# Kernel optimization log

Hardware: AMD Instinct MI355X
Metric: run time of the kernel (lower is better)

## Reference

```python
import jax, jax.numpy as jnp
import numpy as np

B, D, T, K = 32768, 1024, 100, 4  # batch, input_dim, num_trees, 2**(tree_depth-1)

def setup_inputs() -> dict:
    key = jax.random.key(0)
    k1, k2, k3, k4, k5 = jax.random.split(key, 5)
    s1 = 1.0 / np.sqrt(D)
    s2 = 1.0 / np.sqrt(K)
    return {
        "x": jax.random.normal(k1, (B, D), dtype=jnp.float32),
        "W1": jax.random.uniform(k2, (T, K, D), jnp.float32, -s1, s1),  # per-tree first Linear
        "b1": jax.random.uniform(k3, (T, K), jnp.float32, -s1, s1),
        "final_weight": jnp.full((T,), 1.0 / T, dtype=jnp.float32),
        "fc_w": jax.random.uniform(k4, (2, K), jnp.float32, -s2, s2),
        "fc_b": jax.random.uniform(k5, (2,), jnp.float32, -s2, s2),
    }

def reference(x, W1, b1, final_weight, fc_w, fc_b):
    # split_probs for all trees at once: [B, T, K]
    split = jnp.einsum("bd,tkd->btk", x, W1) + b1[None, :, :]
    leaf = jax.nn.sigmoid(split)  # tree[1] is Sigmoid applied to split_probs
    # sum(split.unsqueeze(1)*leaf.unsqueeze(2), -1) == leaf * sum_k(split)
    tree_out = leaf * jnp.sum(split, axis=-1, keepdims=True)  # [B, T, K]
    weighted = jnp.einsum("btk,t->bk", tree_out, final_weight)  # [B, K]
    logits = weighted @ fc_w.T + fc_b  # [B, 2]
    return logits
```

## Files before the change

### kernel.cpp

```cpp
#include <hip/hip_runtime.h>
#include <hip/hip_bf16.h>


typedef __bf16 bf16x8 __attribute__((ext_vector_type(8)));
typedef float f32x4 __attribute__((ext_vector_type(4)));

#define B_ROWS 32768
#define D_DIM  1024
#define N_COLS 400
#define NPAD   512
#define BM     64
#define BK     32
#define NCHUNK 32
#define THREADS 512
#define NTPW 4
#define MT   4

__device__ __forceinline__ unsigned short f2bf(float f) {
    unsigned int u = __float_as_uint(f);
    u += 0x7FFFu + ((u >> 16) & 1u);
    return (unsigned short)(u >> 16);
}
__device__ __forceinline__ unsigned int pk2(float a, float b) {
    return (unsigned int)f2bf(a) | ((unsigned int)f2bf(b) << 16);
}
__device__ __forceinline__ uint4 cvt8u(float4 a, float4 b) {
    uint4 u;
    u.x = pk2(a.x, a.y); u.y = pk2(a.z, a.w);
    u.z = pk2(b.x, b.y); u.w = pk2(b.z, b.w);
    return u;
}
__device__ __forceinline__ bf16x8 cvt8(float4 a, float4 b) {
    return __builtin_bit_cast(bf16x8, cvt8u(a, b));
}

__global__ void cvt_pad_bf16_kernel(const float* __restrict__ in,
                                    unsigned short* __restrict__ out) {
    size_t i = ((size_t)blockIdx.x * 256 + threadIdx.x) * 8;
    if (i < (size_t)N_COLS * D_DIM) {
        float4 v0 = *reinterpret_cast<const float4*>(in + i);
        float4 v1 = *reinterpret_cast<const float4*>(in + i + 4);
        *reinterpret_cast<uint4*>(out + i) = cvt8u(v0, v1);
    } else {
        uint4 z; z.x = z.y = z.z = z.w = 0u;
        *reinterpret_cast<uint4*>(out + i) = z;
    }
}

__device__ __forceinline__ void gl_lds16(const unsigned short* g,
                                         unsigned short* l) {
    __builtin_amdgcn_global_load_lds(
        (const __attribute__((address_space(1))) unsigned int*)g,
        (__attribute__((address_space(3))) unsigned int*)l,
        16, 0, 0);
}

#define FOR_N_(OP, m) OP(m,0) OP(m,1) OP(m,2) OP(m,3)
#define FOR_MN(OP) FOR_N_(OP,0) FOR_N_(OP,1) FOR_N_(OP,2) FOR_N_(OP,3)

#define DECL_ACC(m,n) f32x4 acc##m##n = {};
#define MFMA_MN(m,n) acc##m##n = __builtin_amdgcn_mfma_f32_16x16x32_bf16( \
        afr##m, bfr##n, acc##m##n, 0, 0, 0);

template <int MODE>
__global__ __launch_bounds__(THREADS, 2) void xgb_v13(
    const float* __restrict__ x,
    const void*  __restrict__ b_any,
    const float* __restrict__ b1,
    const float* __restrict__ fw,
    const float* __restrict__ fcw,
    const float* __restrict__ fcb,
    float* __restrict__ out)
{
    __shared__ __align__(16) unsigned short Abuf[2][BM * BK];
    __shared__ __align__(16) unsigned short Bbuf[2][NPAD * BK];
    __shared__ float Pbuf[BM * 8 * 2];

    const int tid  = threadIdx.x;
    const int wave = tid >> 6;
    const int lane = tid & 63;
    const int quad = lane >> 4;
    const int l15  = lane & 15;
    const int nf   = wave;
    const int row0 = blockIdx.x * BM;

    FOR_MN(DECL_ACC)

    if (MODE == 0) {
        const unsigned short* w1b = (const unsigned short*)b_any;

#define BDECL(t) const unsigned short* bsrc##t; int bdst##t; \
        { const int s_ = wave + 8 * (t); const int rb_ = s_ * 16 + (lane >> 2); \
          const int cc_ = ((lane & 3) - (rb_ >> 1)) & 3; \
          bsrc##t = w1b + (size_t)rb_ * D_DIM + cc_ * 8; \
          bdst##t = s_ * 512; }
        BDECL(0) BDECL(1) BDECL(2) BDECL(3)

#define STAGEB(kc, Bb) do { \
        gl_lds16(bsrc0 + (kc), (Bb) + bdst0); \
        gl_lds16(bsrc1 + (kc), (Bb) + bdst1); \
        gl_lds16(bsrc2 + (kc), (Bb) + bdst2); \
        gl_lds16(bsrc3 + (kc), (Bb) + bdst3); } while (0)

        const int slot = tid & 255;
        const int r0a = slot >> 2, c0a = slot & 3;
        const float* asrc0 = x + (size_t)(row0 + r0a) * D_DIM + c0a * 8;
        const int adst0 = r0a * 32 + ((c0a + (r0a >> 1)) & 3) * 8;
        float4 a0lo, a0hi, a1lo, a1hi;

#define LOADA0(kc) do { \
        a0lo = *reinterpret_cast<const float4*>(asrc0 + (kc));     \
        a0hi = *reinterpret_cast<const float4*>(asrc0 + (kc) + 4); } while (0)
#define LOADA1(kc) do { \
        a1lo = *reinterpret_cast<const float4*>(asrc0 + (kc));     \
        a1hi = *reinterpret_cast<const float4*>(asrc0 + (kc) + 4); } while (0)
#define WRITEA0(Ab) do { \
        *reinterpret_cast<uint4*>((Ab) + adst0) = cvt8u(a0lo, a0hi); } while (0)
#define WRITEA1(Ab) do { \
        *reinterpret_cast<uint4*>((Ab) + adst0) = cvt8u(a1lo, a1hi); } while (0)

#define LOAD_AFR(m) { const int row_ = (m) * 16 + l15; \
        const int p_ = (quad + (row_ >> 1)) & 3; \
        afr##m = *reinterpret_cast<const bf16x8*>(Ab_ + row_ * 32 + p_ * 8); }
#define LOAD_BFR(n) { const int row_ = (nf * NTPW + (n)) * 16 + l15; \
        const int p_ = (quad + (row_ >> 1)) & 3; \
        bfr##n = *reinterpret_cast<const bf16x8*>(Bb_ + row_ * 32 + p_ * 8); }

        STAGEB(0, Bbuf[0]);
        __builtin_amdgcn_sched_barrier(0);
        LOADA0(0);
        WRITEA0(Abuf[0]);
        __builtin_amdgcn_sched_barrier(0);
        LOADA1(BK);

        #pragma unroll 1
        for (int c = 0; c < NCHUNK; ++c) {
            const int cur = c & 1;
            const unsigned short* Ab_ = Abuf[cur];
            const unsigned short* Bb_ = Bbuf[cur];
            if (c == NCHUNK - 1) {
                asm volatile("s_waitcnt vmcnt(0)" ::: "memory");
            } else {
                asm volatile("s_waitcnt vmcnt(2)" ::: "memory");
            }
            asm volatile("s_waitcnt lgkmcnt(0)" ::: "memory");
            __builtin_amdgcn_s_barrier();
            __builtin_amdgcn_sched_barrier(0);
            if (c + 1 < NCHUNK) {
                STAGEB((c + 1) * BK, Bbuf[1 - cur]);
                __builtin_amdgcn_sched_barrier(0);
                if (c + 2 < NCHUNK) {
                    if (cur == 0) LOADA0((c + 2) * BK);
                    else          LOADA1((c + 2) * BK);
                }
                __builtin_amdgcn_sched_barrier(0);
            }
            {
                bf16x8 afr0, afr1, afr2, afr3;
                bf16x8 bfr0, bfr1, bfr2, bfr3;
                LOAD_AFR(0) LOAD_AFR(1) LOAD_AFR(2) LOAD_AFR(3)
                LOAD_BFR(0) LOAD_BFR(1) LOAD_BFR(2) LOAD_BFR(3)
                FOR_MN(MFMA_MN)
            }
            if (c + 1 < NCHUNK) {
                if (cur == 0) WRITEA1(Abuf[1]);
                else          WRITEA0(Abuf[0]);
            }
        }
    } else {
        const float* af = x + (size_t)(row0 + l15) * D_DIM + quad * 8;
#define PBF(n) const float* pbf##n; { \
        int r_ = (nf * NTPW + (n)) * 16 + l15; if (r_ > N_COLS - 1) r_ = 0; \
        pbf##n = (const float*)b_any + (size_t)r_ * D_DIM + quad * 8; }
        PBF(0) PBF(1) PBF(2) PBF(3)
        for (int step = 0; step < NCHUNK; ++step) {
            const int off = step * BK;
            bf16x8 afr0, afr1, afr2, afr3;
            bf16x8 bfr0, bfr1, bfr2, bfr3;
#define LAF2(m) afr##m = cvt8( \
            *reinterpret_cast<const float4*>(af + (size_t)(m) * 16 * D_DIM + off), \
            *reinterpret_cast<const float4*>(af + (size_t)(m) * 16 * D_DIM + off + 4));
#define LBF2(n) bfr##n = cvt8( \
            *reinterpret_cast<const float4*>(pbf##n + off), \
            *reinterpret_cast<const float4*>(pbf##n + off + 4));
            LAF2(0) LAF2(1) LAF2(2) LAF2(3)
            LBF2(0) LBF2(1) LBF2(2) LBF2(3)
            FOR_MN(MFMA_MN)
        }
    }

    const float fcw0 = fcw[l15 & 3];
    const float fcw1 = fcw[4 + (l15 & 3)];

#define PRE_N(n) \
    const int  col##n  = (nf * NTPW + (n)) * 16 + l15; \
    const bool ok##n   = (col##n < N_COLS); \
    const float bias##n = ok##n ? b1[ok##n ? col##n : 0] : 0.0f; \
    const float tw##n   = ok##n ? fw[ok##n ? (col##n >> 2) : 0] : 0.0f;
    PRE_N(0) PRE_N(1) PRE_N(2) PRE_N(3)

#define EPI_TERM(m,r,n) { \
        const float split_ = acc##m##n[r] + bias##n; \
        float s_ = split_; \
        s_ += __shfl_xor(s_, 1); \
        s_ += __shfl_xor(s_, 2); \
        const float leaf_ = 1.0f / (1.0f + __expf(-split_)); \
        const float val_ = tw##n * leaf_ * s_; \
        q0 += val_ * fcw0; q1 += val_ * fcw1; }

#define EPI_ONE(m,r) { \
        float q0 = 0.f, q1 = 0.f; \
        EPI_TERM(m,r,0) EPI_TERM(m,r,1) EPI_TERM(m,r,2) EPI_TERM(m,r,3) \
        q0 += __shfl_xor(q0, 1); q0 += __shfl_xor(q0, 2); \
        q0 += __shfl_xor(q0, 4); q0 += __shfl_xor(q0, 8); \
        q1 += __shfl_xor(q1, 1); q1 += __shfl_xor(q1, 2); \
        q1 += __shfl_xor(q1, 4); q1 += __shfl_xor(q1, 8); \
        const int row_ = (m) * 16 + quad * 4 + (r);            \
        if (l15 == 0) Pbuf[(row_ * 8 + nf) * 2 + 0] = q0; \
        if (l15 == 1) Pbuf[(row_ * 8 + nf) * 2 + 1] = q1; }

#define EPI_M(m) EPI_ONE(m,0) EPI_ONE(m,1) EPI_ONE(m,2) EPI_ONE(m,3)
    EPI_M(0) EPI_M(1) EPI_M(2) EPI_M(3)

    __syncthreads();

    if (tid < 2 * BM) {
        const int r = tid >> 1, j = tid & 1;
        float s = fcb[j];
        #pragma unroll
        for (int w = 0; w < 8; ++w)
            s += Pbuf[(r * 8 + w) * 2 + j];
        out[(row0 + r) * 2 + j] = s;
    }
}

extern "C" void kernel_launch(void* const* d_in, const int* in_sizes, int n_in,
                              void* d_out, int out_size, void* d_ws, size_t ws_size,
                              hipStream_t stream) {
    const float* x   = (const float*)d_in[0];
    const float* W1  = (const float*)d_in[1];
    const float* b1  = (const float*)d_in[2];
    const float* fw  = (const float*)d_in[3];
    const float* fcw = (const float*)d_in[4];
    const float* fcb = (const float*)d_in[5];
    float* out = (float*)d_out;

    const size_t pad_elems = (size_t)NPAD * D_DIM;
    if (ws_size >= pad_elems * sizeof(unsigned short)) {
        unsigned short* w1b = (unsigned short*)d_ws;
        cvt_pad_bf16_kernel<<<(int)(pad_elems / 2048), 256, 0, stream>>>(W1, w1b);
        xgb_v13<0><<<B_ROWS / BM, THREADS, 0, stream>>>(
            x, (const void*)w1b, b1, fw, fcw, fcb, out);
    } else {
        xgb_v13<2><<<B_ROWS / BM, THREADS, 0, stream>>>(
            x, (const void*)W1, b1, fw, fcw, fcb, out);
    }
}
```

Before: 276.2 us.

## Enlarge block tile to 128x448 with 64-wide K chunks and 2x4 wave grid

Each block now covers 128 rows and 64-wide K chunks, instead of 64 rows and 32-wide chunks. The eight waves form a 2x4 grid, with each wave computing 4x7 MFMA tiles over a W1 pad shrunk from 512 to 448 columns. This is meant to cut W1 staging per output row, drop most of the wasted padded columns, and halve the number of loop iterations and barriers. The LDS swizzles are rewritten for 64-wide rows, and the x conversion stores now sit before the MFMA loop. The cost is a much larger LDS footprint (about 148 KB) that likely allows only one block per CU, plus higher register pressure from 28 accumulators.

New measurement: 229.4 us. -16.9%, faster.

```diff
diff --git a/kernel.cpp b/kernel.cpp
--- a/kernel.cpp
+++ b/kernel.cpp
@@ -8,12 +8,12 @@
 #define B_ROWS 32768
 #define D_DIM  1024
 #define N_COLS 400
-#define NPAD   512
-#define BM     64
-#define BK     32
-#define NCHUNK 32
+#define NPAD   448
+#define BM     128
+#define BK     64
+#define NCHUNK 16
 #define THREADS 512
-#define NTPW 4
+#define NTPW 7
 #define MT   4
 
 __device__ __forceinline__ unsigned short f2bf(float f) {
@@ -55,7 +55,7 @@
         16, 0, 0);
 }
 
-#define FOR_N_(OP, m) OP(m,0) OP(m,1) OP(m,2) OP(m,3)
+#define FOR_N_(OP, m) OP(m,0) OP(m,1) OP(m,2) OP(m,3) OP(m,4) OP(m,5) OP(m,6)
 #define FOR_MN(OP) FOR_N_(OP,0) FOR_N_(OP,1) FOR_N_(OP,2) FOR_N_(OP,3)
 
 #define DECL_ACC(m,n) f32x4 acc##m##n = {};
@@ -63,7 +63,7 @@
         afr##m, bfr##n, acc##m##n, 0, 0, 0);
 
 template <int MODE>
-__global__ __launch_bounds__(THREADS, 2) void xgb_v13(
+__global__ __launch_bounds__(THREADS, 2) void xgb_v14(
     const float* __restrict__ x,
     const void*  __restrict__ b_any,
     const float* __restrict__ b1,
@@ -74,14 +74,15 @@
 {
     __shared__ __align__(16) unsigned short Abuf[2][BM * BK];
     __shared__ __align__(16) unsigned short Bbuf[2][NPAD * BK];
-    __shared__ float Pbuf[BM * 8 * 2];
+    __shared__ float Pbuf[BM * 4 * 2];
 
     const int tid  = threadIdx.x;
     const int wave = tid >> 6;
     const int lane = tid & 63;
     const int quad = lane >> 4;
     const int l15  = lane & 15;
-    const int nf   = wave;
+    const int mh   = wave >> 2;
+    const int nf   = wave & 3;
     const int row0 = blockIdx.x * BM;
 
     FOR_MN(DECL_ACC)
@@ -90,48 +91,59 @@
         const unsigned short* w1b = (const unsigned short*)b_any;
 
 #define BDECL(t) const unsigned short* bsrc##t; int bdst##t; \
-        { const int s_ = wave + 8 * (t); const int rb_ = s_ * 16 + (lane >> 2); \
-          const int cc_ = ((lane & 3) - (rb_ >> 1)) & 3; \
-          bsrc##t = w1b + (size_t)rb_ * D_DIM + cc_ * 8; \
+        { const int s_ = wave + 8 * (t); const int rr_ = lane >> 3; \
+          const int cc_ = ((lane & 7) - rr_) & 7; \
+          bsrc##t = w1b + (size_t)(s_ * 8 + rr_) * D_DIM + cc_ * 8; \
           bdst##t = s_ * 512; }
-        BDECL(0) BDECL(1) BDECL(2) BDECL(3)
+        BDECL(0) BDECL(1) BDECL(2) BDECL(3) BDECL(4) BDECL(5) BDECL(6)
 
 #define STAGEB(kc, Bb) do { \
         gl_lds16(bsrc0 + (kc), (Bb) + bdst0); \
         gl_lds16(bsrc1 + (kc), (Bb) + bdst1); \
         gl_lds16(bsrc2 + (kc), (Bb) + bdst2); \
-        gl_lds16(bsrc3 + (kc), (Bb) + bdst3); } while (0)
-
-        const int slot = tid & 255;
-        const int r0a = slot >> 2, c0a = slot & 3;
+        gl_lds16(bsrc3 + (kc), (Bb) + bdst3); \
+        gl_lds16(bsrc4 + (kc), (Bb) + bdst4); \
+        gl_lds16(bsrc5 + (kc), (Bb) + bdst5); \
+        gl_lds16(bsrc6 + (kc), (Bb) + bdst6); } while (0)
+
+        const int r0a = tid >> 3, c0a = tid & 7;
         const float* asrc0 = x + (size_t)(row0 + r0a) * D_DIM + c0a * 8;
-        const int adst0 = r0a * 32 + ((c0a + (r0a >> 1)) & 3) * 8;
-        float4 a0lo, a0hi, a1lo, a1hi;
-
-#define LOADA0(kc) do { \
-        a0lo = *reinterpret_cast<const float4*>(asrc0 + (kc));     \
-        a0hi = *reinterpret_cast<const float4*>(asrc0 + (kc) + 4); } while (0)
-#define LOADA1(kc) do { \
-        a1lo = *reinterpret_cast<const float4*>(asrc0 + (kc));     \
-        a1hi = *reinterpret_cast<const float4*>(asrc0 + (kc) + 4); } while (0)
-#define WRITEA0(Ab) do { \
-        *reinterpret_cast<uint4*>((Ab) + adst0) = cvt8u(a0lo, a0hi); } while (0)
-#define WRITEA1(Ab) do { \
-        *reinterpret_cast<uint4*>((Ab) + adst0) = cvt8u(a1lo, a1hi); } while (0)
-
-#define LOAD_AFR(m) { const int row_ = (m) * 16 + l15; \
-        const int p_ = (quad + (row_ >> 1)) & 3; \
-        afr##m = *reinterpret_cast<const bf16x8*>(Ab_ + row_ * 32 + p_ * 8); }
+        const float* asrc1 = asrc0 + (size_t)64 * D_DIM;
+        const int adst0 = r0a * 64 + ((c0a + r0a) & 7) * 8;
+        float4 aX0lo, aX0hi, aX1lo, aX1hi;
+        float4 aY0lo, aY0hi, aY1lo, aY1hi;
+
+#define LOADA_X(kc) do { \
+        aX0lo = *reinterpret_cast<const float4*>(asrc0 + (kc));     \
+        aX0hi = *reinterpret_cast<const float4*>(asrc0 + (kc) + 4); \
+        aX1lo = *reinterpret_cast<const float4*>(asrc1 + (kc));     \
+        aX1hi = *reinterpret_cast<const float4*>(asrc1 + (kc) + 4); } while (0)
+#define LOADA_Y(kc) do { \
+        aY0lo = *reinterpret_cast<const float4*>(asrc0 + (kc));     \
+        aY0hi = *reinterpret_cast<const float4*>(asrc0 + (kc) + 4); \
+        aY1lo = *reinterpret_cast<const float4*>(asrc1 + (kc));     \
+        aY1hi = *reinterpret_cast<const float4*>(asrc1 + (kc) + 4); } while (0)
+#define WRITEA_X(Ab) do { \
+        *reinterpret_cast<uint4*>((Ab) + adst0)        = cvt8u(aX0lo, aX0hi); \
+        *reinterpret_cast<uint4*>((Ab) + adst0 + 4096) = cvt8u(aX1lo, aX1hi); \
+        } while (0)
+#define WRITEA_Y(Ab) do { \
+        *reinterpret_cast<uint4*>((Ab) + adst0)        = cvt8u(aY0lo, aY0hi); \
+        *reinterpret_cast<uint4*>((Ab) + adst0 + 4096) = cvt8u(aY1lo, aY1hi); \
+        } while (0)
+
+#define LOAD_AFR(m) { const int row_ = mh * 64 + (m) * 16 + l15; \
+        const int p_ = (quad + h * 4 + row_) & 7; \
+        afr##m = *reinterpret_cast<const bf16x8*>(Ab_ + row_ * 64 + p_ * 8); }
 #define LOAD_BFR(n) { const int row_ = (nf * NTPW + (n)) * 16 + l15; \
-        const int p_ = (quad + (row_ >> 1)) & 3; \
-        bfr##n = *reinterpret_cast<const bf16x8*>(Bb_ + row_ * 32 + p_ * 8); }
-
+        const int p_ = (quad + h * 4 + row_) & 7; \
+        bfr##n = *reinterpret_cast<const bf16x8*>(Bb_ + row_ * 64 + p_ * 8); }
+
+        LOADA_X(0);
+        WRITEA_X(Abuf[0]);
         STAGEB(0, Bbuf[0]);
         __builtin_amdgcn_sched_barrier(0);
-        LOADA0(0);
-        WRITEA0(Abuf[0]);
-        __builtin_amdgcn_sched_barrier(0);
-        LOADA1(BK);
+        LOADA_Y(BK);
 
         #pragma unroll 1
         for (int c = 0; c < NCHUNK; ++c) {
@@ -141,7 +153,7 @@
             if (c == NCHUNK - 1) {
                 asm volatile("s_waitcnt vmcnt(0)" ::: "memory");
             } else {
-                asm volatile("s_waitcnt vmcnt(2)" ::: "memory");
+                asm volatile("s_waitcnt vmcnt(4)" ::: "memory");
             }
             asm volatile("s_waitcnt lgkmcnt(0)" ::: "memory");
             __builtin_amdgcn_s_barrier();
@@ -149,34 +161,34 @@
             if (c + 1 < NCHUNK) {
                 STAGEB((c + 1) * BK, Bbuf[1 - cur]);
                 __builtin_amdgcn_sched_barrier(0);
+                if (cur == 0) WRITEA_Y(Abuf[1]);
+                else          WRITEA_X(Abuf[0]);
                 if (c + 2 < NCHUNK) {
-                    if (cur == 0) LOADA0((c + 2) * BK);
-                    else          LOADA1((c + 2) * BK);
+                    if (cur == 0) LOADA_X((c + 2) * BK);
+                    else          LOADA_Y((c + 2) * BK);
                 }
                 __builtin_amdgcn_sched_barrier(0);
             }
-            {
+            #pragma unroll
+            for (int h = 0; h < 2; ++h) {
                 bf16x8 afr0, afr1, afr2, afr3;
-                bf16x8 bfr0, bfr1, bfr2, bfr3;
+                bf16x8 bfr0, bfr1, bfr2, bfr3, bfr4, bfr5, bfr6;
                 LOAD_AFR(0) LOAD_AFR(1) LOAD_AFR(2) LOAD_AFR(3)
                 LOAD_BFR(0) LOAD_BFR(1) LOAD_BFR(2) LOAD_BFR(3)
+                LOAD_BFR(4) LOAD_BFR(5) LOAD_BFR(6)
                 FOR_MN(MFMA_MN)
-            }
-            if (c + 1 < NCHUNK) {
-                if (cur == 0) WRITEA1(Abuf[1]);
-                else          WRITEA0(Abuf[0]);
             }
         }
     } else {
-        const float* af = x + (size_t)(row0 + l15) * D_DIM + quad * 8;
+        const float* af = x + (size_t)(row0 + mh * 64 + l15) * D_DIM + quad * 8;
 #define PBF(n) const float* pbf##n; { \
         int r_ = (nf * NTPW + (n)) * 16 + l15; if (r_ > N_COLS - 1) r_ = 0; \
         pbf##n = (const float*)b_any + (size_t)r_ * D_DIM + quad * 8; }
-        PBF(0) PBF(1) PBF(2) PBF(3)
-        for (int step = 0; step < NCHUNK; ++step) {
-            const int off = step * BK;
+        PBF(0) PBF(1) PBF(2) PBF(3) PBF(4) PBF(5) PBF(6)
+        for (int step = 0; step < 32; ++step) {
+            const int off = step * 32;
             bf16x8 afr0, afr1, afr2, afr3;
-            bf16x8 bfr0, bfr1, bfr2, bfr3;
+            bf16x8 bfr0, bfr1, bfr2, bfr3, bfr4, bfr5, bfr6;
 #define LAF2(m) afr##m = cvt8( \
             *reinterpret_cast<const float4*>(af + (size_t)(m) * 16 * D_DIM + off), \
             *reinterpret_cast<const float4*>(af + (size_t)(m) * 16 * D_DIM + off + 4));
@@ -184,7 +196,7 @@
             *reinterpret_cast<const float4*>(pbf##n + off), \
             *reinterpret_cast<const float4*>(pbf##n + off + 4));
             LAF2(0) LAF2(1) LAF2(2) LAF2(3)
-            LBF2(0) LBF2(1) LBF2(2) LBF2(3)
+            LBF2(0) LBF2(1) LBF2(2) LBF2(3) LBF2(4) LBF2(5) LBF2(6)
             FOR_MN(MFMA_MN)
         }
     }
@@ -197,7 +209,7 @@
     const bool ok##n   = (col##n < N_COLS); \
     const float bias##n = ok##n ? b1[ok##n ? col##n : 0] : 0.0f; \
     const float tw##n   = ok##n ? fw[ok##n ? (col##n >> 2) : 0] : 0.0f;
-    PRE_N(0) PRE_N(1) PRE_N(2) PRE_N(3)
+    PRE_N(0) PRE_N(1) PRE_N(2) PRE_N(3) PRE_N(4) PRE_N(5) PRE_N(6)
 
 #define EPI_TERM(m,r,n) { \
         const float split_ = acc##m##n[r] + bias##n; \
@@ -211,13 +223,14 @@
 #define EPI_ONE(m,r) { \
         float q0 = 0.f, q1 = 0.f; \
         EPI_TERM(m,r,0) EPI_TERM(m,r,1) EPI_TERM(m,r,2) EPI_TERM(m,r,3) \
+        EPI_TERM(m,r,4) EPI_TERM(m,r,5) EPI_TERM(m,r,6) \
         q0 += __shfl_xor(q0, 1); q0 += __shfl_xor(q0, 2); \
         q0 += __shfl_xor(q0, 4); q0 += __shfl_xor(q0, 8); \
         q1 += __shfl_xor(q1, 1); q1 += __shfl_xor(q1, 2); \
         q1 += __shfl_xor(q1, 4); q1 += __shfl_xor(q1, 8); \
-        const int row_ = (m) * 16 + quad * 4 + (r);            \
-        if (l15 == 0) Pbuf[(row_ * 8 + nf) * 2 + 0] = q0; \
-        if (l15 == 1) Pbuf[(row_ * 8 + nf) * 2 + 1] = q1; }
+        const int row_ = mh * 64 + (m) * 16 + quad * 4 + (r);    \
+        if (l15 == 0) Pbuf[(row_ * 4 + nf) * 2 + 0] = q0; \
+        if (l15 == 1) Pbuf[(row_ * 4 + nf) * 2 + 1] = q1; }
 
 #define EPI_M(m) EPI_ONE(m,0) EPI_ONE(m,1) EPI_ONE(m,2) EPI_ONE(m,3)
     EPI_M(0) EPI_M(1) EPI_M(2) EPI_M(3)
@@ -228,8 +241,8 @@
         const int r = tid >> 1, j = tid & 1;
         float s = fcb[j];
         #pragma unroll
-        for (int w = 0; w < 8; ++w)
-            s += Pbuf[(r * 8 + w) * 2 + j];
+        for (int w = 0; w < 4; ++w)
+            s += Pbuf[(r * 4 + w) * 2 + j];
         out[(row0 + r) * 2 + j] = s;
     }
 }
@@ -249,10 +262,10 @@
     if (ws_size >= pad_elems * sizeof(unsigned short)) {
         unsigned short* w1b = (unsigned short*)d_ws;
         cvt_pad_bf16_kernel<<<(int)(pad_elems / 2048), 256, 0, stream>>>(W1, w1b);
-        xgb_v13<0><<<B_ROWS / BM, THREADS, 0, stream>>>(
+        xgb_v14<0><<<B_ROWS / BM, THREADS, 0, stream>>>(
             x, (const void*)w1b, b1, fw, fcw, fcb, out);
     } else {
-        xgb_v13<2><<<B_ROWS / BM, THREADS, 0, stream>>>(
+        xgb_v14<2><<<B_ROWS / BM, THREADS, 0, stream>>>(
             x, (const void*)W1, b1, fw, fcw, fcb, out);
     }
 }
```

## Split output columns across two blocks and combine partial logits atomically

Applied to the files above, without the earlier changes.

The 400 tree columns are split into two 224-wide halves, each handled by its own 256-thread block, so the grid doubles and the padded width shrinks from 512 to 448. Each wave now computes a 32x112 tile, and the per-block partial logits are added into a zero-initialised output with atomicAdd, with each half contributing half the bias. The hand-tuned vmcnt waits and the two-deep A prefetch are replaced with a simple __syncthreads single-stage prefetch. The intent is less wasted padding work and more resident blocks per CU. In exchange the x tile is read twice, the change adds a memset launch and atomics, and it gives up the finer load/compute overlap.

Measured after the change: 270.7 us. 2.0% less time.

```diff
diff --git a/kernel.cpp b/kernel.cpp
--- a/kernel.cpp
+++ b/kernel.cpp
@@ -8,13 +8,14 @@
 #define B_ROWS 32768
 #define D_DIM  1024
 #define N_COLS 400
-#define NPAD   512
+#define NPAD   448
 #define BM     64
+#define BN     224
 #define BK     32
 #define NCHUNK 32
-#define THREADS 512
-#define NTPW 4
-#define MT   4
+#define THREADS 256
+#define NTPW 7
+#define MT   2
 
 __device__ __forceinline__ unsigned short f2bf(float f) {
     unsigned int u = __float_as_uint(f);
@@ -55,15 +56,15 @@
         16, 0, 0);
 }
 
-#define FOR_N_(OP, m) OP(m,0) OP(m,1) OP(m,2) OP(m,3)
-#define FOR_MN(OP) FOR_N_(OP,0) FOR_N_(OP,1) FOR_N_(OP,2) FOR_N_(OP,3)
+#define FOR_N_(OP, m) OP(m,0) OP(m,1) OP(m,2) OP(m,3) OP(m,4) OP(m,5) OP(m,6)
+#define FOR_MN(OP) FOR_N_(OP,0) FOR_N_(OP,1)
 
 #define DECL_ACC(m,n) f32x4 acc##m##n = {};
 #define MFMA_MN(m,n) acc##m##n = __builtin_amdgcn_mfma_f32_16x16x32_bf16( \
         afr##m, bfr##n, acc##m##n, 0, 0, 0);
 
 template <int MODE>
-__global__ __launch_bounds__(THREADS, 2) void xgb_v13(
+__global__ __launch_bounds__(THREADS, 3) void xgb_v15(
     const float* __restrict__ x,
     const void*  __restrict__ b_any,
     const float* __restrict__ b1,
@@ -73,16 +74,20 @@
     float* __restrict__ out)
 {
     __shared__ __align__(16) unsigned short Abuf[2][BM * BK];
-    __shared__ __align__(16) unsigned short Bbuf[2][NPAD * BK];
-    __shared__ float Pbuf[BM * 8 * 2];
+    __shared__ __align__(16) unsigned short Bbuf[2][BN * BK];
+    __shared__ float Pbuf[BM * 2 * 2];
 
     const int tid  = threadIdx.x;
     const int wave = tid >> 6;
     const int lane = tid & 63;
     const int quad = lane >> 4;
     const int l15  = lane & 15;
-    const int nf   = wave;
-    const int row0 = blockIdx.x * BM;
+    const int mh   = wave >> 1;
+    const int nf   = wave & 1;
+    const int mb   = blockIdx.x >> 1;
+    const int nh   = blockIdx.x & 1;
+    const int row0 = mb * BM;
+    const int bcol0 = nh * BN;
 
     FOR_MN(DECL_ACC)
 
@@ -90,101 +95,82 @@
         const unsigned short* w1b = (const unsigned short*)b_any;
 
 #define BDECL(t) const unsigned short* bsrc##t; int bdst##t; \
-        { const int s_ = wave + 8 * (t); const int rb_ = s_ * 16 + (lane >> 2); \
-          const int cc_ = ((lane & 3) - (rb_ >> 1)) & 3; \
-          bsrc##t = w1b + (size_t)rb_ * D_DIM + cc_ * 8; \
-          bdst##t = s_ * 512; }
+        { const int s_ = wave + 4 * (t); \
+          const int rb_ = s_ * 16 + (lane >> 2); \
+          const int rc_ = (s_ < 14) ? rb_ : 0;         \
+          const int cc_ = ((lane & 3) - (rc_ >> 1)) & 3; \
+          bsrc##t = w1b + (size_t)(bcol0 + rc_) * D_DIM + cc_ * 8; \
+          bdst##t = (s_ < 14 ? s_ : 0) * 512; }
         BDECL(0) BDECL(1) BDECL(2) BDECL(3)
 
 #define STAGEB(kc, Bb) do { \
         gl_lds16(bsrc0 + (kc), (Bb) + bdst0); \
         gl_lds16(bsrc1 + (kc), (Bb) + bdst1); \
         gl_lds16(bsrc2 + (kc), (Bb) + bdst2); \
-        gl_lds16(bsrc3 + (kc), (Bb) + bdst3); } while (0)
-
-        const int slot = tid & 255;
-        const int r0a = slot >> 2, c0a = slot & 3;
+        if (wave < 2) gl_lds16(bsrc3 + (kc), (Bb) + bdst3); } while (0)
+
+        const int r0a = tid >> 2, c0a = tid & 3;
         const float* asrc0 = x + (size_t)(row0 + r0a) * D_DIM + c0a * 8;
         const int adst0 = r0a * 32 + ((c0a + (r0a >> 1)) & 3) * 8;
-        float4 a0lo, a0hi, a1lo, a1hi;
-
-#define LOADA0(kc) do { \
-        a0lo = *reinterpret_cast<const float4*>(asrc0 + (kc));     \
-        a0hi = *reinterpret_cast<const float4*>(asrc0 + (kc) + 4); } while (0)
-#define LOADA1(kc) do { \
-        a1lo = *reinterpret_cast<const float4*>(asrc0 + (kc));     \
-        a1hi = *reinterpret_cast<const float4*>(asrc0 + (kc) + 4); } while (0)
-#define WRITEA0(Ab) do { \
-        *reinterpret_cast<uint4*>((Ab) + adst0) = cvt8u(a0lo, a0hi); } while (0)
-#define WRITEA1(Ab) do { \
-        *reinterpret_cast<uint4*>((Ab) + adst0) = cvt8u(a1lo, a1hi); } while (0)
-
-#define LOAD_AFR(m) { const int row_ = (m) * 16 + l15; \
+        float4 areg0, areg1;
+
+#define LOADA(kc) do { \
+        areg0 = *reinterpret_cast<const float4*>(asrc0 + (kc));     \
+        areg1 = *reinterpret_cast<const float4*>(asrc0 + (kc) + 4); } while (0)
+#define WRITEA(Ab) do { \
+        *reinterpret_cast<uint4*>((Ab) + adst0) = cvt8u(areg0, areg1); \
+        } while (0)
+
+#define LOAD_AFR(m) { const int row_ = mh * 32 + (m) * 16 + l15; \
         const int p_ = (quad + (row_ >> 1)) & 3; \
         afr##m = *reinterpret_cast<const bf16x8*>(Ab_ + row_ * 32 + p_ * 8); }
 #define LOAD_BFR(n) { const int row_ = (nf * NTPW + (n)) * 16 + l15; \
         const int p_ = (quad + (row_ >> 1)) & 3; \
         bfr##n = *reinterpret_cast<const bf16x8*>(Bb_ + row_ * 32 + p_ * 8); }
 
+        LOADA(0);
         STAGEB(0, Bbuf[0]);
-        __builtin_amdgcn_sched_barrier(0);
-        LOADA0(0);
-        WRITEA0(Abuf[0]);
-        __builtin_amdgcn_sched_barrier(0);
-        LOADA1(BK);
+        WRITEA(Abuf[0]);
 
         #pragma unroll 1
         for (int c = 0; c < NCHUNK; ++c) {
             const int cur = c & 1;
             const unsigned short* Ab_ = Abuf[cur];
             const unsigned short* Bb_ = Bbuf[cur];
-            if (c == NCHUNK - 1) {
-                asm volatile("s_waitcnt vmcnt(0)" ::: "memory");
-            } else {
-                asm volatile("s_waitcnt vmcnt(2)" ::: "memory");
-            }
-            asm volatile("s_waitcnt lgkmcnt(0)" ::: "memory");
-            __builtin_amdgcn_s_barrier();
-            __builtin_amdgcn_sched_barrier(0);
+            __syncthreads();
             if (c + 1 < NCHUNK) {
+                LOADA((c + 1) * BK);
                 STAGEB((c + 1) * BK, Bbuf[1 - cur]);
-                __builtin_amdgcn_sched_barrier(0);
-                if (c + 2 < NCHUNK) {
-                    if (cur == 0) LOADA0((c + 2) * BK);
-                    else          LOADA1((c + 2) * BK);
-                }
-                __builtin_amdgcn_sched_barrier(0);
             }
             {
-                bf16x8 afr0, afr1, afr2, afr3;
-                bf16x8 bfr0, bfr1, bfr2, bfr3;
-                LOAD_AFR(0) LOAD_AFR(1) LOAD_AFR(2) LOAD_AFR(3)
+                bf16x8 afr0, afr1;
+                bf16x8 bfr0, bfr1, bfr2, bfr3, bfr4, bfr5, bfr6;
+                LOAD_AFR(0) LOAD_AFR(1)
                 LOAD_BFR(0) LOAD_BFR(1) LOAD_BFR(2) LOAD_BFR(3)
+                LOAD_BFR(4) LOAD_BFR(5) LOAD_BFR(6)
                 FOR_MN(MFMA_MN)
             }
-            if (c + 1 < NCHUNK) {
-                if (cur == 0) WRITEA1(Abuf[1]);
-                else          WRITEA0(Abuf[0]);
-            }
+            if (c + 1 < NCHUNK) WRITEA(Abuf[1 - cur]);
         }
     } else {
-        const float* af = x + (size_t)(row0 + l15) * D_DIM + quad * 8;
+        const float* af = x + (size_t)(row0 + mh * 32 + l15) * D_DIM + quad * 8;
 #define PBF(n) const float* pbf##n; { \
-        int r_ = (nf * NTPW + (n)) * 16 + l15; if (r_ > N_COLS - 1) r_ = 0; \
+        int r_ = bcol0 + (nf * NTPW + (n)) * 16 + l15; \
+        if (r_ > N_COLS - 1) r_ = 0; \
         pbf##n = (const float*)b_any + (size_t)r_ * D_DIM + quad * 8; }
-        PBF(0) PBF(1) PBF(2) PBF(3)
+        PBF(0) PBF(1) PBF(2) PBF(3) PBF(4) PBF(5) PBF(6)
         for (int step = 0; step < NCHUNK; ++step) {
             const int off = step * BK;
-            bf16x8 afr0, afr1, afr2, afr3;
-            bf16x8 bfr0, bfr1, bfr2, bfr3;
+            bf16x8 afr0, afr1;
+            bf16x8 bfr0, bfr1, bfr2, bfr3, bfr4, bfr5, bfr6;
 #define LAF2(m) afr##m = cvt8( \
             *reinterpret_cast<const float4*>(af + (size_t)(m) * 16 * D_DIM + off), \
             *reinterpret_cast<const float4*>(af + (size_t)(m) * 16 * D_DIM + off + 4));
 #define LBF2(n) bfr##n = cvt8( \
             *reinterpret_cast<const float4*>(pbf##n + off), \
             *reinterpret_cast<const float4*>(pbf##n + off + 4));
-            LAF2(0) LAF2(1) LAF2(2) LAF2(3)
-            LBF2(0) LBF2(1) LBF2(2) LBF2(3)
+            LAF2(0) LAF2(1)
+            LBF2(0) LBF2(1) LBF2(2) LBF2(3) LBF2(4) LBF2(5) LBF2(6)
             FOR_MN(MFMA_MN)
         }
     }
@@ -193,11 +179,11 @@
     const float fcw1 = fcw[4 + (l15 & 3)];
 
 #define PRE_N(n) \
-    const int  col##n  = (nf * NTPW + (n)) * 16 + l15; \
+    const int  col##n  = bcol0 + (nf * NTPW + (n)) * 16 + l15; \
     const bool ok##n   = (col##n < N_COLS); \
     const float bias##n = ok##n ? b1[ok##n ? col##n : 0] : 0.0f; \
     const float tw##n   = ok##n ? fw[ok##n ? (col##n >> 2) : 0] : 0.0f;
-    PRE_N(0) PRE_N(1) PRE_N(2) PRE_N(3)
+    PRE_N(0) PRE_N(1) PRE_N(2) PRE_N(3) PRE_N(4) PRE_N(5) PRE_N(6)
 
 #define EPI_TERM(m,r,n) { \
         const float split_ = acc##m##n[r] + bias##n; \
@@ -211,26 +197,26 @@
 #define EPI_ONE(m,r) { \
         float q0 = 0.f, q1 = 0.f; \
         EPI_TERM(m,r,0) EPI_TERM(m,r,1) EPI_TERM(m,r,2) EPI_TERM(m,r,3) \
+        EPI_TERM(m,r,4) EPI_TERM(m,r,5) EPI_TERM(m,r,6) \
         q0 += __shfl_xor(q0, 1); q0 += __shfl_xor(q0, 2); \
         q0 += __shfl_xor(q0, 4); q0 += __shfl_xor(q0, 8); \
         q1 += __shfl_xor(q1, 1); q1 += __shfl_xor(q1, 2); \
         q1 += __shfl_xor(q1, 4); q1 += __shfl_xor(q1, 8); \
-        const int row_ = (m) * 16 + quad * 4 + (r);            \
-        if (l15 == 0) Pbuf[(row_ * 8 + nf) * 2 + 0] = q0; \
-        if (l15 == 1) Pbuf[(row_ * 8 + nf) * 2 + 1] = q1; }
+        const int row_ = mh * 32 + (m) * 16 + quad * 4 + (r);    \
+        if (l15 == 0) Pbuf[(row_ * 2 + nf) * 2 + 0] = q0; \
+        if (l15 == 1) Pbuf[(row_ * 2 + nf) * 2 + 1] = q1; }
 
 #define EPI_M(m) EPI_ONE(m,0) EPI_ONE(m,1) EPI_ONE(m,2) EPI_ONE(m,3)
-    EPI_M(0) EPI_M(1) EPI_M(2) EPI_M(3)
+    EPI_M(0) EPI_M(1)
 
     __syncthreads();
 
     if (tid < 2 * BM) {
         const int r = tid >> 1, j = tid & 1;
-        float s = fcb[j];
-        #pragma unroll
-        for (int w = 0; w < 8; ++w)
-            s += Pbuf[(r * 8 + w) * 2 + j];
-        out[(row0 + r) * 2 + j] = s;
+        float s = 0.5f * fcb[j]
+                + Pbuf[(r * 2 + 0) * 2 + j]
+                + Pbuf[(r * 2 + 1) * 2 + j];
+        atomicAdd(&out[(size_t)(row0 + r) * 2 + j], s);
     }
 }
 
@@ -245,14 +231,16 @@
     const float* fcb = (const float*)d_in[5];
     float* out = (float*)d_out;
 
+    hipMemsetAsync(out, 0, (size_t)B_ROWS * 2 * sizeof(float), stream);
+
     const size_t pad_elems = (size_t)NPAD * D_DIM;
     if (ws_size >= pad_elems * sizeof(unsigned short)) {
         unsigned short* w1b = (unsigned short*)d_ws;
         cvt_pad_bf16_kernel<<<(int)(pad_elems / 2048), 256, 0, stream>>>(W1, w1b);
-        xgb_v13<0><<<B_ROWS / BM, THREADS, 0, stream>>>(
+        xgb_v15<0><<<(B_ROWS / BM) * 2, THREADS, 0, stream>>>(
             x, (const void*)w1b, b1, fw, fcw, fcb, out);
     } else {
-        xgb_v13<2><<<B_ROWS / BM, THREADS, 0, stream>>>(
+        xgb_v15<2><<<(B_ROWS / BM) * 2, THREADS, 0, stream>>>(
             x, (const void*)W1, b1, fw, fcw, fcb, out);
     }
 }
```

## Warp-specialize GEMM into producer and consumer waves with 4-slot LDS ring

Applied to the files above, without the earlier changes.

Splits the 8 waves into 4 producer waves that stage x (converted to bf16) and W1 tiles into a 4-deep LDS ring, and 4 consumer waves that run MFMAs. Handshakes use LDS atomic counters and spin-waits instead of block barriers. Padding of the N dimension drops from 512 to 448 columns, so each consumer wave covers 7 column tiles and less padded MFMA work is done. The goal is deeper prefetch and less barrier stall. In exchange, only half the waves issue MFMAs, per-wave register pressure is higher, LDS use grows, and the spin-waits add polling overhead.

After: 268.3 us. 2.9% less time.

```diff
diff --git a/kernel.cpp b/kernel.cpp
--- a/kernel.cpp
+++ b/kernel.cpp
@@ -8,12 +8,13 @@
 #define B_ROWS 32768
 #define D_DIM  1024
 #define N_COLS 400
-#define NPAD   512
+#define NPAD   448
 #define BM     64
 #define BK     32
 #define NCHUNK 32
+#define NSLOT  4
 #define THREADS 512
-#define NTPW 4
+#define NTPW 7
 #define MT   4
 
 __device__ __forceinline__ unsigned short f2bf(float f) {
@@ -55,7 +56,7 @@
         16, 0, 0);
 }
 
-#define FOR_N_(OP, m) OP(m,0) OP(m,1) OP(m,2) OP(m,3)
+#define FOR_N_(OP, m) OP(m,0) OP(m,1) OP(m,2) OP(m,3) OP(m,4) OP(m,5) OP(m,6)
 #define FOR_MN(OP) FOR_N_(OP,0) FOR_N_(OP,1) FOR_N_(OP,2) FOR_N_(OP,3)
 
 #define DECL_ACC(m,n) f32x4 acc##m##n = {};
@@ -63,7 +64,7 @@
         afr##m, bfr##n, acc##m##n, 0, 0, 0);
 
 template <int MODE>
-__global__ __launch_bounds__(THREADS, 2) void xgb_v13(
+__global__ __launch_bounds__(THREADS, 2) void xgb_v17(
     const float* __restrict__ x,
     const void*  __restrict__ b_any,
     const float* __restrict__ b1,
@@ -72,132 +73,149 @@
     const float* __restrict__ fcb,
     float* __restrict__ out)
 {
-    __shared__ __align__(16) unsigned short Abuf[2][BM * BK];
-    __shared__ __align__(16) unsigned short Bbuf[2][NPAD * BK];
-    __shared__ float Pbuf[BM * 8 * 2];
+    __shared__ __align__(16) unsigned short Aslot[NSLOT][BM * BK];
+    __shared__ __align__(16) unsigned short Bslot[NSLOT][NPAD * BK];
+    __shared__ float Pbuf[BM * 4 * 2];
+    __shared__ int prodf[NSLOT];
+    __shared__ int consf[NSLOT];
 
     const int tid  = threadIdx.x;
     const int wave = tid >> 6;
     const int lane = tid & 63;
     const int quad = lane >> 4;
     const int l15  = lane & 15;
-    const int nf   = wave;
     const int row0 = blockIdx.x * BM;
 
-    FOR_MN(DECL_ACC)
-
-    if (MODE == 0) {
+    if (tid < NSLOT) { prodf[tid] = 0; consf[tid] = 0; }
+    __syncthreads();
+
+    if (MODE == 0 && wave < 4) {
         const unsigned short* w1b = (const unsigned short*)b_any;
 
+        const int r0a = tid >> 2, c0a = tid & 3;
+        const float* asrc = x + (size_t)(row0 + r0a) * D_DIM + c0a * 8;
+        const int adst = r0a * 32 + ((c0a + (r0a >> 1)) & 3) * 8;
+
 #define BDECL(t) const unsigned short* bsrc##t; int bdst##t; \
-        { const int s_ = wave + 8 * (t); const int rb_ = s_ * 16 + (lane >> 2); \
+        { const int s_ = wave + 4 * (t); \
+          const int rb_ = s_ * 16 + (lane >> 2); \
           const int cc_ = ((lane & 3) - (rb_ >> 1)) & 3; \
           bsrc##t = w1b + (size_t)rb_ * D_DIM + cc_ * 8; \
           bdst##t = s_ * 512; }
-        BDECL(0) BDECL(1) BDECL(2) BDECL(3)
-
-#define STAGEB(kc, Bb) do { \
-        gl_lds16(bsrc0 + (kc), (Bb) + bdst0); \
-        gl_lds16(bsrc1 + (kc), (Bb) + bdst1); \
-        gl_lds16(bsrc2 + (kc), (Bb) + bdst2); \
-        gl_lds16(bsrc3 + (kc), (Bb) + bdst3); } while (0)
-
-        const int slot = tid & 255;
-        const int r0a = slot >> 2, c0a = slot & 3;
-        const float* asrc0 = x + (size_t)(row0 + r0a) * D_DIM + c0a * 8;
-        const int adst0 = r0a * 32 + ((c0a + (r0a >> 1)) & 3) * 8;
-        float4 a0lo, a0hi, a1lo, a1hi;
-
-#define LOADA0(kc) do { \
-        a0lo = *reinterpret_cast<const float4*>(asrc0 + (kc));     \
-        a0hi = *reinterpret_cast<const float4*>(asrc0 + (kc) + 4); } while (0)
-#define LOADA1(kc) do { \
-        a1lo = *reinterpret_cast<const float4*>(asrc0 + (kc));     \
-        a1hi = *reinterpret_cast<const float4*>(asrc0 + (kc) + 4); } while (0)
-#define WRITEA0(Ab) do { \
-        *reinterpret_cast<uint4*>((Ab) + adst0) = cvt8u(a0lo, a0hi); } while (0)
-#define WRITEA1(Ab) do { \
-        *reinterpret_cast<uint4*>((Ab) + adst0) = cvt8u(a1lo, a1hi); } while (0)
+        BDECL(0) BDECL(1) BDECL(2) BDECL(3) BDECL(4) BDECL(5) BDECL(6)
+
+        float4 aXlo, aXhi, aYlo, aYhi;
+
+#define PISSUE(S, c) do { \
+        unsigned short* Bb_ = Bslot[(c) & 3]; \
+        const int kc_ = (c) * BK; \
+        a##S##lo = *reinterpret_cast<const float4*>(asrc + kc_); \
+        a##S##hi = *reinterpret_cast<const float4*>(asrc + kc_ + 4); \
+        __builtin_amdgcn_sched_barrier(0); \
+        gl_lds16(bsrc0 + kc_, Bb_ + bdst0); \
+        gl_lds16(bsrc1 + kc_, Bb_ + bdst1); \
+        gl_lds16(bsrc2 + kc_, Bb_ + bdst2); \
+        gl_lds16(bsrc3 + kc_, Bb_ + bdst3); \
+        gl_lds16(bsrc4 + kc_, Bb_ + bdst4); \
+        gl_lds16(bsrc5 + kc_, Bb_ + bdst5); \
+        gl_lds16(bsrc6 + kc_, Bb_ + bdst6); \
+        __builtin_amdgcn_sched_barrier(0); \
+        } while (0)
+
+#define PWRITE(S, c) do { \
+        unsigned short* Ab_ = Aslot[(c) & 3]; \
+        *reinterpret_cast<uint4*>(Ab_ + adst) = cvt8u(a##S##lo, a##S##hi); \
+        } while (0)
+
+        PISSUE(X, 0);
+        PISSUE(Y, 1);
+
+        #pragma unroll 1
+        for (int c = 0; c < NCHUNK; ++c) {
+            if (c < NCHUNK - 1) asm volatile("s_waitcnt vmcnt(16)" ::: "memory");
+            else                asm volatile("s_waitcnt vmcnt(7)"  ::: "memory");
+            if (c & 1) PWRITE(Y, c); else PWRITE(X, c);
+            if (c < NCHUNK - 1) asm volatile("s_waitcnt vmcnt(9)" ::: "memory");
+            else                asm volatile("s_waitcnt vmcnt(0)" ::: "memory");
+            asm volatile("s_waitcnt lgkmcnt(0)" ::: "memory");
+            __builtin_amdgcn_sched_barrier(0);
+            if (lane == 0) atomicAdd(&prodf[c & 3], 1);
+            if (c + 2 < NCHUNK) {
+                const int cn = c + 2;
+                const int want = 4 * (cn >> 2);
+                if (want > 0) {
+                    while (((volatile int*)consf)[cn & 3] < want)
+                        __builtin_amdgcn_s_sleep(1);
+                }
+                asm volatile("" ::: "memory");
+                __builtin_amdgcn_sched_barrier(0);
+                if (cn & 1) PISSUE(Y, cn); else PISSUE(X, cn);
+            }
+        }
+    } else if (wave >= 4) {
+        const int cw = wave - 4;
+        FOR_MN(DECL_ACC)
 
 #define LOAD_AFR(m) { const int row_ = (m) * 16 + l15; \
         const int p_ = (quad + (row_ >> 1)) & 3; \
         afr##m = *reinterpret_cast<const bf16x8*>(Ab_ + row_ * 32 + p_ * 8); }
-#define LOAD_BFR(n) { const int row_ = (nf * NTPW + (n)) * 16 + l15; \
+#define LOAD_BFR(n) { const int row_ = (cw * NTPW + (n)) * 16 + l15; \
         const int p_ = (quad + (row_ >> 1)) & 3; \
         bfr##n = *reinterpret_cast<const bf16x8*>(Bb_ + row_ * 32 + p_ * 8); }
 
-        STAGEB(0, Bbuf[0]);
-        __builtin_amdgcn_sched_barrier(0);
-        LOADA0(0);
-        WRITEA0(Abuf[0]);
-        __builtin_amdgcn_sched_barrier(0);
-        LOADA1(BK);
-
-        #pragma unroll 1
-        for (int c = 0; c < NCHUNK; ++c) {
-            const int cur = c & 1;
-            const unsigned short* Ab_ = Abuf[cur];
-            const unsigned short* Bb_ = Bbuf[cur];
-            if (c == NCHUNK - 1) {
-                asm volatile("s_waitcnt vmcnt(0)" ::: "memory");
-            } else {
-                asm volatile("s_waitcnt vmcnt(2)" ::: "memory");
-            }
-            asm volatile("s_waitcnt lgkmcnt(0)" ::: "memory");
-            __builtin_amdgcn_s_barrier();
-            __builtin_amdgcn_sched_barrier(0);
-            if (c + 1 < NCHUNK) {
-                STAGEB((c + 1) * BK, Bbuf[1 - cur]);
+        if (MODE == 0) {
+            #pragma unroll 1
+            for (int c = 0; c < NCHUNK; ++c) {
+                const int s_ = c & 3;
+                const int want = 4 * ((c >> 2) + 1);
+                while (((volatile int*)prodf)[s_] < want)
+                    __builtin_amdgcn_s_sleep(1);
+                asm volatile("" ::: "memory");
                 __builtin_amdgcn_sched_barrier(0);
-                if (c + 2 < NCHUNK) {
-                    if (cur == 0) LOADA0((c + 2) * BK);
-                    else          LOADA1((c + 2) * BK);
-                }
-                __builtin_amdgcn_sched_barrier(0);
-            }
-            {
+                const unsigned short* Ab_ = Aslot[s_];
+                const unsigned short* Bb_ = Bslot[s_];
                 bf16x8 afr0, afr1, afr2, afr3;
-                bf16x8 bfr0, bfr1, bfr2, bfr3;
+                bf16x8 bfr0, bfr1, bfr2, bfr3, bfr4, bfr5, bfr6;
                 LOAD_AFR(0) LOAD_AFR(1) LOAD_AFR(2) LOAD_AFR(3)
                 LOAD_BFR(0) LOAD_BFR(1) LOAD_BFR(2) LOAD_BFR(3)
+                LOAD_BFR(4) LOAD_BFR(5) LOAD_BFR(6)
+                FOR_MN(MFMA_MN)
+                asm volatile("s_waitcnt lgkmcnt(0)" ::: "memory");
+                __builtin_amdgcn_sched_barrier(0);
+                if (lane == 0) atomicAdd(&consf[s_], 1);
+            }
+        } else {
+            const float* af = x + (size_t)(row0 + l15) * D_DIM + quad * 8;
+#define PBF(n) const float* pbf##n; { \
+            int r_ = (cw * NTPW + (n)) * 16 + l15; \
+            if (r_ > N_COLS - 1) r_ = 0; \
+            pbf##n = (const float*)b_any + (size_t)r_ * D_DIM + quad * 8; }
+            PBF(0) PBF(1) PBF(2) PBF(3) PBF(4) PBF(5) PBF(6)
+            for (int step = 0; step < NCHUNK; ++step) {
+                const int off = step * BK;
+                bf16x8 afr0, afr1, afr2, afr3;
+                bf16x8 bfr0, bfr1, bfr2, bfr3, bfr4, bfr5, bfr6;
+#define LAF2(m) afr##m = cvt8( \
+                *reinterpret_cast<const float4*>(af + (size_t)(m) * 16 * D_DIM + off), \
+                *reinterpret_cast<const float4*>(af + (size_t)(m) * 16 * D_DIM + off + 4));
+#define LBF2(n) bfr##n = cvt8( \
+                *reinterpret_cast<const float4*>(pbf##n + off), \
+                *reinterpret_cast<const float4*>(pbf##n + off + 4));
+                LAF2(0) LAF2(1) LAF2(2) LAF2(3)
+                LBF2(0) LBF2(1) LBF2(2) LBF2(3) LBF2(4) LBF2(5) LBF2(6)
                 FOR_MN(MFMA_MN)
             }
-            if (c + 1 < NCHUNK) {
-                if (cur == 0) WRITEA1(Abuf[1]);
-                else          WRITEA0(Abuf[0]);
-            }
         }
-    } else {
-        const float* af = x + (size_t)(row0 + l15) * D_DIM + quad * 8;
-#define PBF(n) const float* pbf##n; { \
-        int r_ = (nf * NTPW + (n)) * 16 + l15; if (r_ > N_COLS - 1) r_ = 0; \
-        pbf##n = (const float*)b_any + (size_t)r_ * D_DIM + quad * 8; }
-        PBF(0) PBF(1) PBF(2) PBF(3)
-        for (int step = 0; step < NCHUNK; ++step) {
-            const int off = step * BK;
-            bf16x8 afr0, afr1, afr2, afr3;
-            bf16x8 bfr0, bfr1, bfr2, bfr3;
-#define LAF2(m) afr##m = cvt8( \
-            *reinterpret_cast<const float4*>(af + (size_t)(m) * 16 * D_DIM + off), \
-            *reinterpret_cast<const float4*>(af + (size_t)(m) * 16 * D_DIM + off + 4));
-#define LBF2(n) bfr##n = cvt8( \
-            *reinterpret_cast<const float4*>(pbf##n + off), \
-            *reinterpret_cast<const float4*>(pbf##n + off + 4));
-            LAF2(0) LAF2(1) LAF2(2) LAF2(3)
-            LBF2(0) LBF2(1) LBF2(2) LBF2(3)
-            FOR_MN(MFMA_MN)
-        }
-    }
-
-    const float fcw0 = fcw[l15 & 3];
-    const float fcw1 = fcw[4 + (l15 & 3)];
+
+        const float fcw0 = fcw[l15 & 3];
+        const float fcw1 = fcw[4 + (l15 & 3)];
 
 #define PRE_N(n) \
-    const int  col##n  = (nf * NTPW + (n)) * 16 + l15; \
-    const bool ok##n   = (col##n < N_COLS); \
-    const float bias##n = ok##n ? b1[ok##n ? col##n : 0] : 0.0f; \
-    const float tw##n   = ok##n ? fw[ok##n ? (col##n >> 2) : 0] : 0.0f;
-    PRE_N(0) PRE_N(1) PRE_N(2) PRE_N(3)
+        const int  col##n  = (cw * NTPW + (n)) * 16 + l15; \
+        const bool ok##n   = (col##n < N_COLS); \
+        const float bias##n = ok##n ? b1[ok##n ? col##n : 0] : 0.0f; \
+        const float tw##n   = ok##n ? fw[ok##n ? (col##n >> 2) : 0] : 0.0f;
+        PRE_N(0) PRE_N(1) PRE_N(2) PRE_N(3) PRE_N(4) PRE_N(5) PRE_N(6)
 
 #define EPI_TERM(m,r,n) { \
         const float split_ = acc##m##n[r] + bias##n; \
@@ -211,16 +229,18 @@
 #define EPI_ONE(m,r) { \
         float q0 = 0.f, q1 = 0.f; \
         EPI_TERM(m,r,0) EPI_TERM(m,r,1) EPI_TERM(m,r,2) EPI_TERM(m,r,3) \
+        EPI_TERM(m,r,4) EPI_TERM(m,r,5) EPI_TERM(m,r,6) \
         q0 += __shfl_xor(q0, 1); q0 += __shfl_xor(q0, 2); \
         q0 += __shfl_xor(q0, 4); q0 += __shfl_xor(q0, 8); \
         q1 += __shfl_xor(q1, 1); q1 += __shfl_xor(q1, 2); \
         q1 += __shfl_xor(q1, 4); q1 += __shfl_xor(q1, 8); \
         const int row_ = (m) * 16 + quad * 4 + (r);            \
-        if (l15 == 0) Pbuf[(row_ * 8 + nf) * 2 + 0] = q0; \
-        if (l15 == 1) Pbuf[(row_ * 8 + nf) * 2 + 1] = q1; }
+        if (l15 == 0) Pbuf[(row_ * 4 + cw) * 2 + 0] = q0; \
+        if (l15 == 1) Pbuf[(row_ * 4 + cw) * 2 + 1] = q1; }
 
 #define EPI_M(m) EPI_ONE(m,0) EPI_ONE(m,1) EPI_ONE(m,2) EPI_ONE(m,3)
-    EPI_M(0) EPI_M(1) EPI_M(2) EPI_M(3)
+        EPI_M(0) EPI_M(1) EPI_M(2) EPI_M(3)
+    }
 
     __syncthreads();
 
@@ -228,9 +248,9 @@
         const int r = tid >> 1, j = tid & 1;
         float s = fcb[j];
         #pragma unroll
-        for (int w = 0; w < 8; ++w)
-            s += Pbuf[(r * 8 + w) * 2 + j];
-        out[(row0 + r) * 2 + j] = s;
+        for (int w = 0; w < 4; ++w)
+            s += Pbuf[(r * 4 + w) * 2 + j];
+        out[(size_t)(row0 + r) * 2 + j] = s;
     }
 }
 
@@ -249,10 +269,10 @@
     if (ws_size >= pad_elems * sizeof(unsigned short)) {
         unsigned short* w1b = (unsigned short*)d_ws;
         cvt_pad_bf16_kernel<<<(int)(pad_elems / 2048), 256, 0, stream>>>(W1, w1b);
-        xgb_v13<0><<<B_ROWS / BM, THREADS, 0, stream>>>(
+        xgb_v17<0><<<B_ROWS / BM, THREADS, 0, stream>>>(
             x, (const void*)w1b, b1, fw, fcw, fcb, out);
     } else {
-        xgb_v13<2><<<B_ROWS / BM, THREADS, 0, stream>>>(
+        xgb_v17<2><<<B_ROWS / BM, THREADS, 0, stream>>>(
             x, (const void*)W1, b1, fw, fcw, fcb, out);
     }
 }
```
